# Performance work log

Measured on AMD Instinct MI355X. Metric: run time of the kernel, lower is better.

## Reference

```python
import jax, jax.numpy as jnp
import numpy as np

EPS = 0.5  # diffusion epsilon from init_kwargs

def setup_inputs() -> dict:
    key = jax.random.key(0)
    k = jax.random.split(key, 7)
    B, N0, N1, n = 1024, 32, 32, 64
    Mu0 = jax.random.normal(k[0], (N0, n), dtype=jnp.float32) * 2.0
    Mu1 = jax.random.normal(k[1], (N1, n), dtype=jnp.float32) * 2.0
    # diagonal covariances must be positive
    S0 = jax.random.uniform(k[2], (N0, n), dtype=jnp.float32, minval=0.1, maxval=1.0)
    S1 = jax.random.uniform(k[3], (N1, n), dtype=jnp.float32, minval=0.1, maxval=1.0)
    Lam = jax.random.uniform(k[4], (N0, N1), dtype=jnp.float32, minval=0.0, maxval=1.0)
    Lam = Lam / Lam.sum()  # transport plan sums to 1
    X = jax.random.normal(k[5], (B, n), dtype=jnp.float32)
    t = jnp.float32(0.3)
    return {"X": X, "Mu0": Mu0, "Mu1": Mu1, "S0": S0, "S1": S1, "Lam": Lam, "t": t}

def reference(X, Mu0, Mu1, S0, S1, Lam, t):
    eps2 = EPS * EPS
    S0e = S0[:, None, :]        # (N0,1,n)
    S1e = S1[None, :, :]        # (1,N1,n)
    Ds = jnp.sqrt(4.0 * S0e * S1e + EPS ** 4)
    Cs = 0.5 * (Ds - eps2)                       # (N0,N1,n)
    mu_t = (1.0 - t) * Mu0[:, None, :] + t * Mu1[None, :, :]  # (N0,N1,n)
    Sigma = (1.0 - t) ** 2 * S0e + t ** 2 * S1e + 2.0 * t * (1.0 - t) * (Cs + 0.5 * eps2)
    # St = Pt - Qt - eps^2 * t
    St = t * S1e + (1.0 - t) * Cs - ((1.0 - t) * S0e + t * Cs) - eps2 * t
    K = St / Sigma                               # (N0,N1,n)
    v = Mu1[None, :, :] - Mu0[:, None, :]        # (N0,N1,n)
    d = X[:, None, None, :] - mu_t               # (B,N0,N1,n)
    U = K * d + v                                # (B,N0,N1,n)
    # diag-Normal log_prob plus n/2*log(2pi) == -0.5*sum(d^2/Sigma + log Sigma)
    logw = -0.5 * jnp.sum(d * d / Sigma + jnp.log(Sigma), axis=-1)  # (B,N0,N1)
    W = jnp.exp(jnp.clip(logw, -50.0, 50.0)) * Lam                  # (B,N0,N1)
    num = jnp.einsum('bijn,bij->bn', U, W)       # (B,n)
    den = jnp.sum(W, axis=(1, 2))[:, None]       # (B,1)
    return num / den
```

## Files before the change

kernel.cpp:

```cpp
#include <hip/hip_runtime.h>
#include <math.h>

#define EPS2f 0.25f
#define EPS4f 0.0625f

__global__ __launch_bounds__(256) void precomp_kernel(
    const float* __restrict__ Mu0, const float* __restrict__ Mu1,
    const float* __restrict__ S0,  const float* __restrict__ S1,
    const float* __restrict__ tptr,
    float2* __restrict__ AB2, float2* __restrict__ KV2,
    float* __restrict__ C0)
{
    const int tid = threadIdx.x;
    const int k   = tid & 63;
    const int ij  = (blockIdx.x << 2) + (tid >> 6);
    const int i   = ij >> 5;
    const int j   = ij & 31;
    const float t   = *tptr;
    const float omt = 1.0f - t;

    const float s0 = S0[i * 64 + k];
    const float s1 = S1[j * 64 + k];
    const float m0 = Mu0[i * 64 + k];
    const float m1 = Mu1[j * 64 + k];

    const float ds  = sqrtf(4.0f * s0 * s1 + EPS4f);
    const float cs  = 0.5f * (ds - EPS2f);
    const float mt  = omt * m0 + t * m1;
    const float sig = omt * omt * s0 + t * t * s1
                    + 2.0f * t * omt * (cs + 0.5f * EPS2f);
    const float isig = 1.0f / sig;
    const float st = t * s1 - omt * s0 + (omt - t) * cs - EPS2f * t;
    const float kk = st * isig;
    const float v  = m1 - m0;

    AB2[((k >> 1) << 11) + (ij << 1) + (k & 1)] = make_float2(isig, 2.0f * mt * isig);
    KV2[((ij >> 1) << 7) + (k << 1) + (ij & 1)] = make_float2(kk, v - kk * mt);

    float c = mt * mt * isig + __logf(sig);
    #pragma unroll
    for (int off = 32; off >= 1; off >>= 1)
        c += __shfl_xor(c, off, 64);
    if (k == 0) C0[ij] = c;
}

__global__ __launch_bounds__(1024) void gmm_main_kernel(
    const float* __restrict__ X,   const float* __restrict__ Lam,
    const float* __restrict__ C0,
    const float4* __restrict__ AB4, const float4* __restrict__ KV4,
    float* __restrict__ out)
{
    __shared__ float4 Xs4[64];
    __shared__ float4 Wl4[1024 * 2];
    __shared__ float  red[16 * 64 * 5];
    __shared__ float  XsT[4 * 64];
    __shared__ float  denp[16 * 4];

    const int tid  = threadIdx.x;
    const int lane = tid & 63;
    const int w    = tid >> 6;
    const int b0   = blockIdx.x << 2;

    if (tid < 256) {
        const int bb = tid >> 6, k = tid & 63;
        const float xv = X[(b0 + bb) * 64 + k];
        ((float*)&Xs4[k])[bb] = xv;
        XsT[bb * 64 + k] = xv;
    }
    __syncthreads();

    const int ij = tid;
    const float c0 = C0[ij];
    const float lm = Lam[ij];
    float qa = 0.f, qb = 0.f, qc = 0.f, qd = 0.f;
    #pragma unroll 8
    for (int k2 = 0; k2 < 32; ++k2) {
        const float4 ab = AB4[(k2 << 10) + ij];
        const float4 x0 = Xs4[2 * k2];
        const float4 x1 = Xs4[2 * k2 + 1];
        qa = fmaf(fmaf(ab.x, x0.x, -ab.y), x0.x, qa);
        qb = fmaf(fmaf(ab.x, x0.y, -ab.y), x0.y, qb);
        qc = fmaf(fmaf(ab.x, x0.z, -ab.y), x0.z, qc);
        qd = fmaf(fmaf(ab.x, x0.w, -ab.y), x0.w, qd);
        qa = fmaf(fmaf(ab.z, x1.x, -ab.w), x1.x, qa);
        qb = fmaf(fmaf(ab.z, x1.y, -ab.w), x1.y, qb);
        qc = fmaf(fmaf(ab.z, x1.z, -ab.w), x1.z, qc);
        qd = fmaf(fmaf(ab.z, x1.w, -ab.w), x1.w, qd);
    }

    #define WCALC(q) (__expf(fminf(fmaxf(-0.5f * ((q) + c0), -50.f), 50.f)) * lm)
    float4 wv4;
    wv4.x = WCALC(qa); wv4.y = WCALC(qb); wv4.z = WCALC(qc); wv4.w = WCALC(qd);
    #undef WCALC
    Wl4[ij * 2] = wv4;

    float d0 = wv4.x, d1 = wv4.y, d2 = wv4.z, d3 = wv4.w;
    #pragma unroll
    for (int off = 32; off >= 1; off >>= 1) {
        d0 += __shfl_xor(d0, off, 64);
        d1 += __shfl_xor(d1, off, 64);
        d2 += __shfl_xor(d2, off, 64);
        d3 += __shfl_xor(d3, off, 64);
    }
    if (lane == 0) {
        denp[w * 4 + 0] = d0; denp[w * 4 + 1] = d1;
        denp[w * 4 + 2] = d2; denp[w * 4 + 3] = d3;
    }

    const float xk0 = XsT[0 * 64 + lane], xk1 = XsT[1 * 64 + lane];
    const float xk2 = XsT[2 * 64 + lane], xk3 = XsT[3 * 64 + lane];
    float n0 = 0.f, n1 = 0.f, n2 = 0.f, n3 = 0.f;
    const int p0 = w << 5;
    #pragma unroll 8
    for (int p = 0; p < 32; ++p) {
        const float4 kv = KV4[((p0 + p) << 6) + lane];
        const float4 we = Wl4[(p0 + p) * 4];
        const float4 wo = Wl4[(p0 + p) * 4 + 2];
        float u;
        u = fmaf(kv.x, xk0, kv.y); n0 = fmaf(we.x, u, n0);
        u = fmaf(kv.x, xk1, kv.y); n1 = fmaf(we.y, u, n1);
        u = fmaf(kv.x, xk2, kv.y); n2 = fmaf(we.z, u, n2);
        u = fmaf(kv.x, xk3, kv.y); n3 = fmaf(we.w, u, n3);
        u = fmaf(kv.z, xk0, kv.w); n0 = fmaf(wo.x, u, n0);
        u = fmaf(kv.z, xk1, kv.w); n1 = fmaf(wo.y, u, n1);
        u = fmaf(kv.z, xk2, kv.w); n2 = fmaf(wo.z, u, n2);
        u = fmaf(kv.z, xk3, kv.w); n3 = fmaf(wo.w, u, n3);
    }
    {
        float* r = &red[(w * 64 + lane) * 5];
        r[0] = n0; r[1] = n1; r[2] = n2; r[3] = n3;
    }
    __syncthreads();

    if (tid < 256) {
        const int bb = tid >> 6, k = tid & 63;
        float s = 0.f, d = 0.f;
        #pragma unroll
        for (int ww = 0; ww < 16; ++ww) {
            s += red[(ww * 64 + k) * 5 + bb];
            d += denp[ww * 4 + bb];
        }
        out[(b0 + bb) * 64 + k] = s / d;
    }
}

extern "C" void kernel_launch(void* const* d_in, const int* in_sizes, int n_in,
                              void* d_out, int out_size, void* d_ws, size_t ws_size,
                              hipStream_t stream) {
    const float* X   = (const float*)d_in[0];
    const float* Mu0 = (const float*)d_in[1];
    const float* Mu1 = (const float*)d_in[2];
    const float* S0  = (const float*)d_in[3];
    const float* S1  = (const float*)d_in[4];
    const float* Lam = (const float*)d_in[5];
    const float* t   = (const float*)d_in[6];
    float* out = (float*)d_out;

    char* ws = (char*)d_ws;
    float2* AB2 = (float2*)(ws);
    float2* KV2 = (float2*)(ws + (512 << 10));
    float*  C0  = (float*)(ws + (1024 << 10));

    precomp_kernel<<<256, 256, 0, stream>>>(Mu0, Mu1, S0, S1, t, AB2, KV2, C0);
    gmm_main_kernel<<<256, 1024, 0, stream>>>(X, Lam, C0,
                                              (const float4*)AB2,
                                              (const float4*)KV2, out);
}
```

Before: 79.40 us.

## Tile main kernel over 32 batch rows and split components across blocks

```diff
diff --git a/kernel.cpp b/kernel.cpp
--- a/kernel.cpp
+++ b/kernel.cpp
@@ -44,104 +44,125 @@
     if (k == 0) C0[ij] = c;
 }
 
-__global__ __launch_bounds__(1024) void gmm_main_kernel(
+__global__ __launch_bounds__(1024, 4) void gmm_main_kernel(
     const float* __restrict__ X,   const float* __restrict__ Lam,
     const float* __restrict__ C0,
-    const float4* __restrict__ AB4, const float4* __restrict__ KV4,
-    float* __restrict__ out)
+    const float4* __restrict__ AB4, const float4* __restrict__ KVP4,
+    float* __restrict__ num_p, float* __restrict__ den_p)
 {
-    __shared__ float4 Xs4[64];
-    __shared__ float4 Wl4[1024 * 2];
-    __shared__ float  red[16 * 64 * 5];
-    __shared__ float  XsT[4 * 64];
-    __shared__ float  denp[16 * 4];
+    __shared__ float Xs[64 * 36];
+    __shared__ float Wl[32 * 128];
 
-    const int tid  = threadIdx.x;
-    const int lane = tid & 63;
-    const int w    = tid >> 6;
-    const int b0   = blockIdx.x << 2;
+    const int tid   = threadIdx.x;
+    const int lane  = tid & 63;
+    const int w     = tid >> 6;
+    const int e     = blockIdx.x & 7;
+    const int chunk = blockIdx.x >> 3;
 
-    if (tid < 256) {
-        const int bb = tid >> 6, k = tid & 63;
-        const float xv = X[(b0 + bb) * 64 + k];
-        ((float*)&Xs4[k])[bb] = xv;
-        XsT[bb * 64 + k] = xv;
+    {
+        int t0 = tid;
+        int row = t0 >> 6, k = t0 & 63;
+        Xs[k * 36 + row] = X[(chunk * 32 + row) * 64 + k];
+        t0 = tid + 1024;
+        row = t0 >> 6; k = t0 & 63;
+        Xs[k * 36 + row] = X[(chunk * 32 + row) * 64 + k];
     }
     __syncthreads();
 
-    const int ij = tid;
-    const float c0 = C0[ij];
-    const float lm = Lam[ij];
-    float qa = 0.f, qb = 0.f, qc = 0.f, qd = 0.f;
+    const int rg   = tid >> 7;
+    const int ij_l = tid & 127;
+    const int ij_g = (e << 7) + ij_l;
+    float q0 = 0.f, q1 = 0.f, q2 = 0.f, q3 = 0.f;
     #pragma unroll 8
     for (int k2 = 0; k2 < 32; ++k2) {
-        const float4 ab = AB4[(k2 << 10) + ij];
-        const float4 x0 = Xs4[2 * k2];
-        const float4 x1 = Xs4[2 * k2 + 1];
-        qa = fmaf(fmaf(ab.x, x0.x, -ab.y), x0.x, qa);
-        qb = fmaf(fmaf(ab.x, x0.y, -ab.y), x0.y, qb);
-        qc = fmaf(fmaf(ab.x, x0.z, -ab.y), x0.z, qc);
-        qd = fmaf(fmaf(ab.x, x0.w, -ab.y), x0.w, qd);
-        qa = fmaf(fmaf(ab.z, x1.x, -ab.w), x1.x, qa);
-        qb = fmaf(fmaf(ab.z, x1.y, -ab.w), x1.y, qb);
-        qc = fmaf(fmaf(ab.z, x1.z, -ab.w), x1.z, qc);
-        qd = fmaf(fmaf(ab.z, x1.w, -ab.w), x1.w, qd);
+        const float4 ab = AB4[(k2 << 10) + ij_g];
+        const float4 x0 = *(const float4*)&Xs[(2 * k2) * 36 + 4 * rg];
+        const float4 x1 = *(const float4*)&Xs[(2 * k2 + 1) * 36 + 4 * rg];
+        q0 = fmaf(fmaf(ab.x, x0.x, -ab.y), x0.x, q0);
+        q1 = fmaf(fmaf(ab.x, x0.y, -ab.y), x0.y, q1);
+        q2 = fmaf(fmaf(ab.x, x0.z, -ab.y), x0.z, q2);
+        q3 = fmaf(fmaf(ab.x, x0.w, -ab.y), x0.w, q3);
+        q0 = fmaf(fmaf(ab.z, x1.x, -ab.w), x1.x, q0);
+        q1 = fmaf(fmaf(ab.z, x1.y, -ab.w), x1.y, q1);
+        q2 = fmaf(fmaf(ab.z, x1.z, -ab.w), x1.z, q2);
+        q3 = fmaf(fmaf(ab.z, x1.w, -ab.w), x1.w, q3);
+    }
+    const float c0 = C0[ij_g];
+    const float lm = Lam[ij_g];
+    #define WCALC(q) (__expf(fminf(fmaxf(-0.5f * ((q) + c0), -50.f), 50.f)) * lm)
+    Wl[(4 * rg + 0) * 128 + ij_l] = WCALC(q0);
+    Wl[(4 * rg + 1) * 128 + ij_l] = WCALC(q1);
+    Wl[(4 * rg + 2) * 128 + ij_l] = WCALC(q2);
+    Wl[(4 * rg + 3) * 128 + ij_l] = WCALC(q3);
+    #undef WCALC
+
+    const int g    = w >> 1;
+    const int half = w & 1;
+    const float x0v = Xs[lane * 36 + 4 * g + 0];
+    const float x1v = Xs[lane * 36 + 4 * g + 1];
+    const float x2v = Xs[lane * 36 + 4 * g + 2];
+    const float x3v = Xs[lane * 36 + 4 * g + 3];
+    float n0 = 0.f, n1 = 0.f, n2 = 0.f, n3 = 0.f;
+    float d0 = 0.f, d1 = 0.f, d2 = 0.f, d3 = 0.f;
+    const int pbase = (e << 6) + (half << 5);
+
+    #pragma unroll 8
+    for (int p = 0; p < 32; ++p) {
+        const float4 kv = KVP4[((pbase + p) << 6) + lane];
+        const int ijp = (half << 6) + 2 * p;
+        const float2 wr0 = *(const float2*)&Wl[(4 * g + 0) * 128 + ijp];
+        const float2 wr1 = *(const float2*)&Wl[(4 * g + 1) * 128 + ijp];
+        const float2 wr2 = *(const float2*)&Wl[(4 * g + 2) * 128 + ijp];
+        const float2 wr3 = *(const float2*)&Wl[(4 * g + 3) * 128 + ijp];
+        float u;
+        u = fmaf(kv.x, x0v, kv.y); n0 = fmaf(wr0.x, u, n0);
+        u = fmaf(kv.z, x0v, kv.w); n0 = fmaf(wr0.y, u, n0);
+        d0 += wr0.x + wr0.y;
+        u = fmaf(kv.x, x1v, kv.y); n1 = fmaf(wr1.x, u, n1);
+        u = fmaf(kv.z, x1v, kv.w); n1 = fmaf(wr1.y, u, n1);
+        d1 += wr1.x + wr1.y;
+        u = fmaf(kv.x, x2v, kv.y); n2 = fmaf(wr2.x, u, n2);
+        u = fmaf(kv.z, x2v, kv.w); n2 = fmaf(wr2.y, u, n2);
+        d2 += wr2.x + wr2.y;
+        u = fmaf(kv.x, x3v, kv.y); n3 = fmaf(wr3.x, u, n3);
+        u = fmaf(kv.z, x3v, kv.w); n3 = fmaf(wr3.y, u, n3);
+        d3 += wr3.x + wr3.y;
     }
 
-    #define WCALC(q) (__expf(fminf(fmaxf(-0.5f * ((q) + c0), -50.f), 50.f)) * lm)
-    float4 wv4;
-    wv4.x = WCALC(qa); wv4.y = WCALC(qb); wv4.z = WCALC(qc); wv4.w = WCALC(qd);
-    #undef WCALC
-    Wl4[ij * 2] = wv4;
+    const int pid = ((e * 32 + chunk) * 16 + w);
+    num_p[(pid * 4 + 0) * 64 + lane] = n0;
+    num_p[(pid * 4 + 1) * 64 + lane] = n1;
+    num_p[(pid * 4 + 2) * 64 + lane] = n2;
+    num_p[(pid * 4 + 3) * 64 + lane] = n3;
+    if (lane == 0) {
+        den_p[pid * 4 + 0] = d0;
+        den_p[pid * 4 + 1] = d1;
+        den_p[pid * 4 + 2] = d2;
+        den_p[pid * 4 + 3] = d3;
+    }
+}
 
-    float d0 = wv4.x, d1 = wv4.y, d2 = wv4.z, d3 = wv4.w;
+__global__ __launch_bounds__(256) void finalize_kernel(
+    const float* __restrict__ num_p, const float* __restrict__ den_p,
+    float* __restrict__ out)
+{
+    const int idx   = blockIdx.x * 256 + threadIdx.x;
+    const int k     = idx & 63;
+    const int b     = idx >> 6;
+    const int chunk = b >> 5;
+    const int row   = b & 31;
+    const int g     = row >> 2, s = row & 3;
+    float sum = 0.f, den = 0.f;
     #pragma unroll
-    for (int off = 32; off >= 1; off >>= 1) {
-        d0 += __shfl_xor(d0, off, 64);
-        d1 += __shfl_xor(d1, off, 64);
-        d2 += __shfl_xor(d2, off, 64);
-        d3 += __shfl_xor(d3, off, 64);
+    for (int e = 0; e < 8; ++e) {
+        #pragma unroll
+        for (int half = 0; half < 2; ++half) {
+            const int pid = ((e * 32 + chunk) * 16 + (g * 2 + half));
+            sum += num_p[(pid * 4 + s) * 64 + k];
+            den += den_p[pid * 4 + s];
+        }
     }
-    if (lane == 0) {
-        denp[w * 4 + 0] = d0; denp[w * 4 + 1] = d1;
-        denp[w * 4 + 2] = d2; denp[w * 4 + 3] = d3;
-    }
-
-    const float xk0 = XsT[0 * 64 + lane], xk1 = XsT[1 * 64 + lane];
-    const float xk2 = XsT[2 * 64 + lane], xk3 = XsT[3 * 64 + lane];
-    float n0 = 0.f, n1 = 0.f, n2 = 0.f, n3 = 0.f;
-    const int p0 = w << 5;
-    #pragma unroll 8
-    for (int p = 0; p < 32; ++p) {
-        const float4 kv = KV4[((p0 + p) << 6) + lane];
-        const float4 we = Wl4[(p0 + p) * 4];
-        const float4 wo = Wl4[(p0 + p) * 4 + 2];
-        float u;
-        u = fmaf(kv.x, xk0, kv.y); n0 = fmaf(we.x, u, n0);
-        u = fmaf(kv.x, xk1, kv.y); n1 = fmaf(we.y, u, n1);
-        u = fmaf(kv.x, xk2, kv.y); n2 = fmaf(we.z, u, n2);
-        u = fmaf(kv.x, xk3, kv.y); n3 = fmaf(we.w, u, n3);
-        u = fmaf(kv.z, xk0, kv.w); n0 = fmaf(wo.x, u, n0);
-        u = fmaf(kv.z, xk1, kv.w); n1 = fmaf(wo.y, u, n1);
-        u = fmaf(kv.z, xk2, kv.w); n2 = fmaf(wo.z, u, n2);
-        u = fmaf(kv.z, xk3, kv.w); n3 = fmaf(wo.w, u, n3);
-    }
-    {
-        float* r = &red[(w * 64 + lane) * 5];
-        r[0] = n0; r[1] = n1; r[2] = n2; r[3] = n3;
-    }
-    __syncthreads();
-
-    if (tid < 256) {
-        const int bb = tid >> 6, k = tid & 63;
-        float s = 0.f, d = 0.f;
-        #pragma unroll
-        for (int ww = 0; ww < 16; ++ww) {
-            s += red[(ww * 64 + k) * 5 + bb];
-            d += denp[ww * 4 + bb];
-        }
-        out[(b0 + bb) * 64 + k] = s / d;
-    }
+    out[idx] = sum / den;
 }
 
 extern "C" void kernel_launch(void* const* d_in, const int* in_sizes, int n_in,
@@ -157,12 +178,15 @@
     float* out = (float*)d_out;
 
     char* ws = (char*)d_ws;
-    float2* AB2 = (float2*)(ws);
-    float2* KV2 = (float2*)(ws + (512 << 10));
-    float*  C0  = (float*)(ws + (1024 << 10));
+    float2* AB2  = (float2*)(ws);
+    float2* KV2  = (float2*)(ws + (512 << 10));
+    float*  C0   = (float*)(ws + (1024 << 10));
+    float*  nump = (float*)(ws + 1310720u);
+    float*  denp = (float*)(ws + 5767168u);
 
     precomp_kernel<<<256, 256, 0, stream>>>(Mu0, Mu1, S0, S1, t, AB2, KV2, C0);
     gmm_main_kernel<<<256, 1024, 0, stream>>>(X, Lam, C0,
                                               (const float4*)AB2,
-                                              (const float4*)KV2, out);
+                                              (const float4*)KV2, nump, denp);
+    finalize_kernel<<<256, 256, 0, stream>>>(nump, denp, out);
 }
```

Result: slower. 90.52 us (+14.0%).
